# Kernel tuning notes

Measured on AMD Instinct MI355X. Metric: run time of the kernel, lower is better.

## Reference

```python
import jax, jax.numpy as jnp
import numpy as np

B, S, D = 64, 512, 512  # bias broadcast and final bmm force S == input_dim == dim_v
DK, DV = 512, 512


def setup_inputs() -> dict:
    key = jax.random.key(0)
    ks = jax.random.split(key, 16)
    sc = 0.02
    inp = {
        "sent_emb": jax.random.normal(ks[0], (B, S, D), jnp.float32),
        "pos_emb": jax.random.normal(ks[1], (B, S, D), jnp.float32),
        "branch_emb": jax.random.normal(ks[2], (B, S, D), jnp.float32),
        # Linear weights stored torch-style: [out, in]
        "Wq": jax.random.normal(ks[3], (DK, D), jnp.float32) * sc,
        "bq": jnp.zeros((DK,), jnp.float32),
        "Wk": jax.random.normal(ks[4], (DK, D), jnp.float32) * sc,
        "bk": jnp.zeros((DK,), jnp.float32),
        "Wv": jax.random.normal(ks[5], (DV, D), jnp.float32) * sc,
        "bv": jnp.zeros((DV,), jnp.float32),
        "Wpq": jax.random.normal(ks[6], (D, D), jnp.float32) * sc,
        "bpq": jnp.zeros((D,), jnp.float32),
        "Wpk": jax.random.normal(ks[7], (D, D), jnp.float32) * sc,
        "bpk": jnp.zeros((D,), jnp.float32),
        "bias": jax.random.normal(ks[8], (D,), jnp.float32) * sc,
    }
    return inp


def reference(sent_emb, pos_emb, branch_emb, Wq, bq, Wk, bk, Wv, bv, Wpq, bpq, Wpk, bpk, bias):
    d = sent_emb.shape[-1]
    norm = 1.0 / jnp.sqrt(jnp.asarray(2.0 * d, sent_emb.dtype))
    # projections (torch Linear: x @ W.T + b)
    Q = sent_emb @ Wq.T + bq          # [B,S,DK]
    K = sent_emb @ Wk.T + bk          # [B,S,DK]
    V = sent_emb @ Wv.T + bv          # [B,S,DV]
    Uq = pos_emb @ Wpq.T + bpq        # [B,S,D]
    Uk = pos_emb @ Wpk.T + bpk        # [B,S,D]
    text_score = jnp.einsum('bsd,btd->bst', Q, K) * norm   # [B,S,S]
    pos_score = jnp.einsum('bsd,btd->bst', Uq, Uk) * norm  # [B,S,S]
    att = text_score + pos_score + bias                    # bias [D] broadcasts over last axis (S==D)
    att_softmax = jax.nn.softmax(att, axis=2)
    # torch.bmm(att, V.permute(0,2,1)): out[b,i,j] = sum_t att[b,i,t] * V[b,j,t]
    output = jnp.einsum('bit,bjt->bij', att_softmax, V)    # [B,S,S] (DV==S)
    return (att_softmax, output)
```

## Files before the change

### kernel.cpp

```cpp
#include <hip/hip_runtime.h>

typedef unsigned short u16;
typedef unsigned int   u32;
typedef __bf16 bf16x8 __attribute__((ext_vector_type(8)));
typedef float  f32x4  __attribute__((ext_vector_type(4)));

#define BATCH 64
#define SEQ   512
#define BSS   (64 * 512 * 512)
#define MTOT  (64 * 512)

__device__ __forceinline__ u16 f2bf(float f) {
  u32 u = __builtin_bit_cast(u32, f);
  u += 0x7FFFu + ((u >> 16) & 1u);
  return (u16)(u >> 16);
}

__device__ __forceinline__ void gl16(const void* g, void* l) {
  __builtin_amdgcn_global_load_lds(
      (__attribute__((address_space(1))) void*)g,
      (__attribute__((address_space(3))) void*)l,
      16, 0, 0);
}

__global__ __launch_bounds__(256) void cvt2_bf16_kernel(
    const float* __restrict__ in0, u16* __restrict__ out0,
    const float* __restrict__ in1, u16* __restrict__ out1, int n8) {
  int i = blockIdx.x * 256 + threadIdx.x;
  const float* in = in0;
  u16* out = out0;
  if (i >= n8) { i -= n8; in = in1; out = out1; }
  const float4* p = reinterpret_cast<const float4*>(in) + (size_t)i * 2;
  float4 x = p[0], y = p[1];
  uint4 r;
  r.x = (u32)f2bf(x.x) | ((u32)f2bf(x.y) << 16);
  r.y = (u32)f2bf(x.z) | ((u32)f2bf(x.w) << 16);
  r.z = (u32)f2bf(y.x) | ((u32)f2bf(y.y) << 16);
  r.w = (u32)f2bf(y.z) | ((u32)f2bf(y.w) << 16);
  reinterpret_cast<uint4*>(out)[i] = r;
}

__global__ __launch_bounds__(256) void pack_w_kernel(
    const float* __restrict__ wq, const float* __restrict__ wk,
    const float* __restrict__ wv, const float* __restrict__ wpq,
    const float* __restrict__ wpk, u16* __restrict__ wc1, u16* __restrict__ wc2) {
  int i = blockIdx.x * 256 + threadIdx.x;
  int which = i >> 18;
  int off = i & 262143;
  const float* src = which == 0 ? wq : which == 1 ? wk : which == 2 ? wv
                   : which == 3 ? wpq : wpk;
  u16 h = f2bf(src[off]);
  if (which < 3) wc1[(size_t)which * 262144 + off] = h;
  else           wc2[(size_t)(which - 3) * 262144 + off] = h;
}

__global__ __launch_bounds__(256) void pack_bias_kernel(
    const float* __restrict__ bq, const float* __restrict__ bk,
    const float* __restrict__ bv, const float* __restrict__ bpq,
    const float* __restrict__ bpk, float* __restrict__ b1, float* __restrict__ b2) {
  int i = blockIdx.x * 256 + threadIdx.x;
  if (i < 1536) {
    b1[i] = i < 512 ? bq[i] : i < 1024 ? bk[i - 512] : bv[i - 1024];
  } else {
    int j = i - 1536;
    b2[j] = j < 512 ? bpq[j] : bpk[j - 512];
  }
}

template <int MODE>
__global__ __launch_bounds__(512, 2) void gemm256(
    const u16* __restrict__ A, const u16* __restrict__ Bm,
    u16* __restrict__ U0, u16* __restrict__ U1, u16* __restrict__ U2,
    const float* __restrict__ bias, float* __restrict__ F) {
  __shared__ u16 lsA[256 * 32];
  __shared__ u16 lsB[128 * 32];

  const int t = threadIdx.x;
  const int z = blockIdx.z;
  const int m0 = blockIdx.y * 256;
  const int n0 = blockIdx.x * 128;
  const int K = 512;

  const u16* Ab = A + (MODE == 2 ? (size_t)z * 262144 : 0);
  const u16* Bb = Bm + (MODE == 2 ? (size_t)z * 262144 : 0);
  float* Fb = (MODE == 2) ? (F + (size_t)z * 262144) : F;

  const int srow = t >> 2;
  const int scol = (t & 3) * 8;
  const u16* gA = Ab + (size_t)(m0 + srow) * K + scol;
  const u16* gB = Bb + (size_t)(n0 + srow) * K + scol;
  const size_t rskip = (size_t)128 * K;
  u16* lA0 = lsA + t * 8;
  u16* lA1 = lsA + 4096 + t * 8;
  u16* lB0 = lsB + t * 8;

  const int l = t & 63;
  const int w = t >> 6;
  const int wm = (w & 3) * 64;
  const int wn = (w >> 2) * 64;
  const int fr = l & 15;
  const int fk = (l >> 4) * 8;

  f32x4 acc[4][4];
#pragma unroll
  for (int i = 0; i < 4; ++i)
#pragma unroll
    for (int j = 0; j < 4; ++j) acc[i][j] = (f32x4){0.f, 0.f, 0.f, 0.f};

  for (int k0 = 0; k0 < K; k0 += 32) {
    gl16(gA + k0, lA0);
    gl16(gA + rskip + k0, lA1);
    gl16(gB + k0, lB0);
    __syncthreads();
    bf16x8 af[4], bfg[4];
#pragma unroll
    for (int mt = 0; mt < 4; ++mt)
      af[mt] = *reinterpret_cast<const bf16x8*>(&lsA[(wm + mt * 16 + fr) * 32 + fk]);
#pragma unroll
    for (int nt = 0; nt < 4; ++nt)
      bfg[nt] = *reinterpret_cast<const bf16x8*>(&lsB[(wn + nt * 16 + fr) * 32 + fk]);
#pragma unroll
    for (int mt = 0; mt < 4; ++mt)
#pragma unroll
      for (int nt = 0; nt < 4; ++nt)
        acc[mt][nt] = __builtin_amdgcn_mfma_f32_16x16x32_bf16(
            af[mt], bfg[nt], acc[mt][nt], 0, 0, 0);
    __syncthreads();
  }

  const int cr = (l >> 4) * 4;
  const int cc = l & 15;
#pragma unroll
  for (int mt = 0; mt < 4; ++mt) {
#pragma unroll
    for (int nt = 0; nt < 4; ++nt) {
      const int col = n0 + wn + nt * 16 + cc;
#pragma unroll
      for (int r = 0; r < 4; ++r) {
        const int row = m0 + wm + mt * 16 + cr + r;
        float v = acc[mt][nt][r];
        if (MODE == 2) {
          Fb[(size_t)row * 512 + col] = v;
        } else {
          v += bias[col];
          u16 h = f2bf(v);
          const int which = col >> 9, c = col & 511;
          if (MODE == 0) {
            if (which == 0)      U0[(size_t)row * 1024 + c] = h;
            else if (which == 1) U1[(size_t)row * 1024 + c] = h;
            else                 U2[(size_t)row * 512 + c] = h;
          } else {
            if (which == 0) U0[(size_t)row * 1024 + 512 + c] = h;
            else            U1[(size_t)row * 1024 + 512 + c] = h;
          }
        }
      }
    }
  }
}

__global__ __launch_bounds__(512, 4) void score_softmax(
    const u16* __restrict__ QU, const u16* __restrict__ KU,
    const float* __restrict__ bias, float* __restrict__ attF,
    u16* __restrict__ attB) {
  __shared__ u16 lsA[64 * 256];
  __shared__ float sred[64 * 8];

  const int t = threadIdx.x;
  const int b = blockIdx.x;
  const int rg = blockIdx.y;
  const int l = t & 63;
  const int w = t >> 6;
  const int wn = w * 64;
  const int fr = l & 15;
  const int fkb = (l >> 4) * 16;
  const int cc = l & 15;
  const int cr = (l >> 4) * 4;
  const int sw = (l & 7) << 4;

  const int browA = b * 512 + rg * 64;

  const int stg_colb = ((t & 31) << 4) ^ (((t >> 5) & 7) << 4);
  const char* gAc = (const char*)QU + (size_t)(browA + (t >> 5)) * 2048 + stg_colb;

  const u16* gK = KU + (size_t)(b * 512 + wn + fr) * 1024 + (l >> 4) * 8;

  float bc[4];
#pragma unroll
  for (int nt = 0; nt < 4; ++nt) bc[nt] = bias[wn + nt * 16 + cc];

  f32x4 acc[4][4];
#pragma unroll
  for (int i = 0; i < 4; ++i)
#pragma unroll
    for (int j = 0; j < 4; ++j) acc[i][j] = (f32x4){0.f, 0.f, 0.f, 0.f};

#pragma unroll
  for (int c = 0; c < 4; ++c) {
    __syncthreads();
#pragma unroll
    for (int i = 0; i < 4; ++i)
      gl16(gAc + c * 512 + (size_t)i * 16 * 2048,
           (char*)lsA + t * 16 + (size_t)i * 8192);
    __syncthreads();

#pragma unroll 2
    for (int kk = 0; kk < 8; ++kk) {
      bf16x8 af[4], bfg[4];
#pragma unroll
      for (int nt = 0; nt < 4; ++nt)
        bfg[nt] = *reinterpret_cast<const bf16x8*>(
            gK + (size_t)nt * 16 * 1024 + c * 256 + kk * 32);
#pragma unroll
      for (int mt = 0; mt < 4; ++mt)
        af[mt] = *reinterpret_cast<const bf16x8*>(
            (const char*)lsA + (mt * 16 + fr) * 512 + ((kk * 64 + fkb) ^ sw));
#pragma unroll
      for (int mt = 0; mt < 4; ++mt)
#pragma unroll
        for (int nt = 0; nt < 4; ++nt)
          acc[mt][nt] = __builtin_amdgcn_mfma_f32_16x16x32_bf16(
              af[mt], bfg[nt], acc[mt][nt], 0, 0, 0);
    }
  }

#pragma unroll
  for (int mt = 0; mt < 4; ++mt)
#pragma unroll
    for (int nt = 0; nt < 4; ++nt)
#pragma unroll
      for (int r = 0; r < 4; ++r)
        acc[mt][nt][r] = acc[mt][nt][r] * 0.03125f + bc[nt];

  float rm[4][4];
#pragma unroll
  for (int mt = 0; mt < 4; ++mt)
#pragma unroll
    for (int r = 0; r < 4; ++r) {
      float m = fmaxf(fmaxf(acc[mt][0][r], acc[mt][1][r]),
                      fmaxf(acc[mt][2][r], acc[mt][3][r]));
#pragma unroll
      for (int s = 1; s < 16; s <<= 1) m = fmaxf(m, __shfl_xor(m, s, 64));
      rm[mt][r] = m;
    }
  if (cc == 0) {
#pragma unroll
    for (int mt = 0; mt < 4; ++mt)
#pragma unroll
      for (int r = 0; r < 4; ++r)
        sred[(mt * 16 + cr + r) * 8 + w] = rm[mt][r];
  }
  __syncthreads();
#pragma unroll
  for (int mt = 0; mt < 4; ++mt)
#pragma unroll
    for (int r = 0; r < 4; ++r) {
      const float* p = &sred[(mt * 16 + cr + r) * 8];
      f32x4 a = *reinterpret_cast<const f32x4*>(p);
      f32x4 c = *reinterpret_cast<const f32x4*>(p + 4);
      rm[mt][r] = fmaxf(fmaxf(fmaxf(a[0], a[1]), fmaxf(a[2], a[3])),
                        fmaxf(fmaxf(c[0], c[1]), fmaxf(c[2], c[3])));
    }
  __syncthreads();

  float rs[4][4];
#pragma unroll
  for (int mt = 0; mt < 4; ++mt)
#pragma unroll
    for (int r = 0; r < 4; ++r) {
      float s = 0.f;
#pragma unroll
      for (int nt = 0; nt < 4; ++nt) {
        float e = __expf(acc[mt][nt][r] - rm[mt][r]);
        acc[mt][nt][r] = e;
        s += e;
      }
#pragma unroll
      for (int sh = 1; sh < 16; sh <<= 1) s += __shfl_xor(s, sh, 64);
      rs[mt][r] = s;
    }
  if (cc == 0) {
#pragma unroll
    for (int mt = 0; mt < 4; ++mt)
#pragma unroll
      for (int r = 0; r < 4; ++r)
        sred[(mt * 16 + cr + r) * 8 + w] = rs[mt][r];
  }
  __syncthreads();
#pragma unroll
  for (int mt = 0; mt < 4; ++mt)
#pragma unroll
    for (int r = 0; r < 4; ++r) {
      const float* p = &sred[(mt * 16 + cr + r) * 8];
      f32x4 a = *reinterpret_cast<const f32x4*>(p);
      f32x4 c = *reinterpret_cast<const f32x4*>(p + 4);
      rs[mt][r] = 1.0f / ((a[0] + a[1]) + (a[2] + a[3]) +
                          (c[0] + c[1]) + (c[2] + c[3]));
    }

  float* aF = attF + (size_t)b * 262144 + (size_t)rg * 64 * 512;
  u16* aB = attB + (size_t)b * 262144 + (size_t)rg * 64 * 512;
#pragma unroll
  for (int mt = 0; mt < 4; ++mt)
#pragma unroll
    for (int nt = 0; nt < 4; ++nt)
#pragma unroll
      for (int r = 0; r < 4; ++r) {
        const size_t idx = (size_t)(mt * 16 + cr + r) * 512 + wn + nt * 16 + cc;
        float a = acc[mt][nt][r] * rs[mt][r];
        aF[idx] = a;
        aB[idx] = f2bf(a);
      }
}

extern "C" void kernel_launch(void* const* d_in, const int* in_sizes, int n_in,
                              void* d_out, int out_size, void* d_ws,
                              size_t ws_size, hipStream_t stream) {
  const float* sent = (const float*)d_in[0];
  const float* pos  = (const float*)d_in[1];
  const float* Wq  = (const float*)d_in[3];
  const float* bq  = (const float*)d_in[4];
  const float* Wk  = (const float*)d_in[5];
  const float* bk  = (const float*)d_in[6];
  const float* Wv  = (const float*)d_in[7];
  const float* bv  = (const float*)d_in[8];
  const float* Wpq = (const float*)d_in[9];
  const float* bpq = (const float*)d_in[10];
  const float* Wpk = (const float*)d_in[11];
  const float* bpk = (const float*)d_in[12];
  const float* abias = (const float*)d_in[13];
  float* out = (float*)d_out;

  char* ws = (char*)d_ws;
  u16* Xs   = (u16*)(ws);
  u16* Xp   = (u16*)(ws + 33554432ul);
  u16* QU   = (u16*)(ws + 67108864ul);
  u16* KU   = (u16*)(ws + 134217728ul);
  u16* Vb   = (u16*)(ws + 201326592ul);
  u16* attB = (u16*)(ws + 234881024ul);
  u16* Wc1  = (u16*)(ws + 268435456ul);
  u16* Wc2  = (u16*)(ws + 270008320ul);
  float* b1 = (float*)(ws + 271056896ul);
  float* b2 = (float*)(ws + 271063040ul);

  float* attF = out;
  float* out2 = out + BSS;

  cvt2_bf16_kernel<<<16384, 256, 0, stream>>>(sent, Xs, pos, Xp, MTOT * 512 / 8);
  pack_w_kernel<<<5120, 256, 0, stream>>>(Wq, Wk, Wv, Wpq, Wpk, Wc1, Wc2);
  pack_bias_kernel<<<10, 256, 0, stream>>>(bq, bk, bv, bpq, bpk, b1, b2);

  gemm256<0><<<dim3(12, 128, 1), 512, 0, stream>>>(Xs, Wc1, QU, KU, Vb, b1, nullptr);
  gemm256<1><<<dim3(8, 128, 1), 512, 0, stream>>>(Xp, Wc2, QU, KU, nullptr, b2, nullptr);

  score_softmax<<<dim3(BATCH, 8, 1), 512, 0, stream>>>(QU, KU, abias, attF, attB);

  gemm256<2><<<dim3(4, 2, BATCH), 512, 0, stream>>>(attB, Vb, nullptr, nullptr,
                                                    nullptr, nullptr, out2);

  (void)in_sizes; (void)n_in; (void)out_size; (void)ws_size;
}
```

Measured before the change: 542.9 us.

## Replace LDS-staged GEMM with barrier-free direct global-to-register MFMA loads

Result: slower. 766.3 us (+41.1%).

```diff
diff --git a/kernel.cpp b/kernel.cpp
--- a/kernel.cpp
+++ b/kernel.cpp
@@ -68,38 +68,28 @@
 }
 
 template <int MODE>
-__global__ __launch_bounds__(512, 2) void gemm256(
+__global__ __launch_bounds__(256, 2) void gemm_bfree(
     const u16* __restrict__ A, const u16* __restrict__ Bm,
     u16* __restrict__ U0, u16* __restrict__ U1, u16* __restrict__ U2,
     const float* __restrict__ bias, float* __restrict__ F) {
-  __shared__ u16 lsA[256 * 32];
-  __shared__ u16 lsB[128 * 32];
-
   const int t = threadIdx.x;
   const int z = blockIdx.z;
-  const int m0 = blockIdx.y * 256;
+  const int m0 = blockIdx.y * 128;
   const int n0 = blockIdx.x * 128;
-  const int K = 512;
 
   const u16* Ab = A + (MODE == 2 ? (size_t)z * 262144 : 0);
   const u16* Bb = Bm + (MODE == 2 ? (size_t)z * 262144 : 0);
   float* Fb = (MODE == 2) ? (F + (size_t)z * 262144) : F;
 
-  const int srow = t >> 2;
-  const int scol = (t & 3) * 8;
-  const u16* gA = Ab + (size_t)(m0 + srow) * K + scol;
-  const u16* gB = Bb + (size_t)(n0 + srow) * K + scol;
-  const size_t rskip = (size_t)128 * K;
-  u16* lA0 = lsA + t * 8;
-  u16* lA1 = lsA + 4096 + t * 8;
-  u16* lB0 = lsB + t * 8;
-
   const int l = t & 63;
   const int w = t >> 6;
-  const int wm = (w & 3) * 64;
-  const int wn = (w >> 2) * 64;
+  const int wm = (w & 1) * 64;
+  const int wn = (w >> 1) * 64;
   const int fr = l & 15;
-  const int fk = (l >> 4) * 8;
+  const int fo = (l >> 4) * 8;
+
+  const u16* gA = Ab + (size_t)(m0 + wm + fr) * 512 + fo;
+  const u16* gB = Bb + (size_t)(n0 + wn + fr) * 512 + fo;
 
   f32x4 acc[4][4];
 #pragma unroll
@@ -107,25 +97,38 @@
 #pragma unroll
     for (int j = 0; j < 4; ++j) acc[i][j] = (f32x4){0.f, 0.f, 0.f, 0.f};
 
-  for (int k0 = 0; k0 < K; k0 += 32) {
-    gl16(gA + k0, lA0);
-    gl16(gA + rskip + k0, lA1);
-    gl16(gB + k0, lB0);
-    __syncthreads();
-    bf16x8 af[4], bfg[4];
-#pragma unroll
-    for (int mt = 0; mt < 4; ++mt)
-      af[mt] = *reinterpret_cast<const bf16x8*>(&lsA[(wm + mt * 16 + fr) * 32 + fk]);
-#pragma unroll
-    for (int nt = 0; nt < 4; ++nt)
-      bfg[nt] = *reinterpret_cast<const bf16x8*>(&lsB[(wn + nt * 16 + fr) * 32 + fk]);
+  bf16x8 a0[4], b0[4], a1[4], b1[4];
+#pragma unroll
+  for (int i = 0; i < 4; ++i) {
+    a0[i] = *reinterpret_cast<const bf16x8*>(gA + (size_t)i * 16 * 512);
+    b0[i] = *reinterpret_cast<const bf16x8*>(gB + (size_t)i * 16 * 512);
+  }
+
+  for (int k0 = 0; k0 < 512; k0 += 64) {
+    const int k1 = k0 + 32;
+    const int k2 = (k0 + 64) & 511;
+#pragma unroll
+    for (int i = 0; i < 4; ++i) {
+      a1[i] = *reinterpret_cast<const bf16x8*>(gA + (size_t)i * 16 * 512 + k1);
+      b1[i] = *reinterpret_cast<const bf16x8*>(gB + (size_t)i * 16 * 512 + k1);
+    }
 #pragma unroll
     for (int mt = 0; mt < 4; ++mt)
 #pragma unroll
       for (int nt = 0; nt < 4; ++nt)
         acc[mt][nt] = __builtin_amdgcn_mfma_f32_16x16x32_bf16(
-            af[mt], bfg[nt], acc[mt][nt], 0, 0, 0);
-    __syncthreads();
+            a0[mt], b0[nt], acc[mt][nt], 0, 0, 0);
+#pragma unroll
+    for (int i = 0; i < 4; ++i) {
+      a0[i] = *reinterpret_cast<const bf16x8*>(gA + (size_t)i * 16 * 512 + k2);
+      b0[i] = *reinterpret_cast<const bf16x8*>(gB + (size_t)i * 16 * 512 + k2);
+    }
+#pragma unroll
+    for (int mt = 0; mt < 4; ++mt)
+#pragma unroll
+      for (int nt = 0; nt < 4; ++nt)
+        acc[mt][nt] = __builtin_amdgcn_mfma_f32_16x16x32_bf16(
+            a1[mt], b1[nt], acc[mt][nt], 0, 0, 0);
   }
 
   const int cr = (l >> 4) * 4;
@@ -350,13 +353,13 @@
   pack_w_kernel<<<5120, 256, 0, stream>>>(Wq, Wk, Wv, Wpq, Wpk, Wc1, Wc2);
   pack_bias_kernel<<<10, 256, 0, stream>>>(bq, bk, bv, bpq, bpk, b1, b2);
 
-  gemm256<0><<<dim3(12, 128, 1), 512, 0, stream>>>(Xs, Wc1, QU, KU, Vb, b1, nullptr);
-  gemm256<1><<<dim3(8, 128, 1), 512, 0, stream>>>(Xp, Wc2, QU, KU, nullptr, b2, nullptr);
+  gemm_bfree<0><<<dim3(12, 256, 1), 256, 0, stream>>>(Xs, Wc1, QU, KU, Vb, b1, nullptr);
+  gemm_bfree<1><<<dim3(8, 256, 1), 256, 0, stream>>>(Xp, Wc2, QU, KU, nullptr, b2, nullptr);
 
   score_softmax<<<dim3(BATCH, 8, 1), 512, 0, stream>>>(QU, KU, abias, attF, attB);
 
-  gemm256<2><<<dim3(4, 2, BATCH), 512, 0, stream>>>(attB, Vb, nullptr, nullptr,
-                                                    nullptr, nullptr, out2);
+  gemm_bfree<2><<<dim3(4, 4, BATCH), 256, 0, stream>>>(attB, Vb, nullptr, nullptr,
+                                                       nullptr, nullptr, out2);
 
   (void)in_sizes; (void)n_in; (void)out_size; (void)ws_size;
 }
```

## Double-buffer GEMM LDS tiles with XOR swizzle and XCD-aware block remap

Applied to the files above, without the earlier changes.

Result: faster. 504.0 us (-7.2%).

```diff
diff --git a/kernel.cpp b/kernel.cpp
--- a/kernel.cpp
+++ b/kernel.cpp
@@ -68,38 +68,46 @@
 }
 
 template <int MODE>
-__global__ __launch_bounds__(512, 2) void gemm256(
+__global__ __launch_bounds__(512, 4) void gemm_db(
     const u16* __restrict__ A, const u16* __restrict__ Bm,
     u16* __restrict__ U0, u16* __restrict__ U1, u16* __restrict__ U2,
     const float* __restrict__ bias, float* __restrict__ F) {
-  __shared__ u16 lsA[256 * 32];
-  __shared__ u16 lsB[128 * 32];
+  __shared__ u16 ls[2 * 12288];
 
   const int t = threadIdx.x;
-  const int z = blockIdx.z;
-  const int m0 = blockIdx.y * 256;
-  const int n0 = blockIdx.x * 128;
+
+  const int gx = gridDim.x, gy = gridDim.y;
+  int id = (blockIdx.z * gy + blockIdx.y) * gx + blockIdx.x;
+  const int q = (gx * gy * gridDim.z) >> 3;
+  id = (id & 7) * q + (id >> 3);
+  const int bx = id % gx;
+  const int rem = id / gx;
+  const int by = rem % gy;
+  const int z = rem / gy;
+
+  const int m0 = by * 256;
+  const int n0 = bx * 128;
   const int K = 512;
 
   const u16* Ab = A + (MODE == 2 ? (size_t)z * 262144 : 0);
   const u16* Bb = Bm + (MODE == 2 ? (size_t)z * 262144 : 0);
   float* Fb = (MODE == 2) ? (F + (size_t)z * 262144) : F;
 
-  const int srow = t >> 2;
-  const int scol = (t & 3) * 8;
+  const int u = (t & 7) ^ ((t >> 3) & 7);
+  const int srow = 2 * (t >> 3) + (u & 1);
+  const int scol = (u >> 1) * 8;
   const u16* gA = Ab + (size_t)(m0 + srow) * K + scol;
   const u16* gB = Bb + (size_t)(n0 + srow) * K + scol;
-  const size_t rskip = (size_t)128 * K;
-  u16* lA0 = lsA + t * 8;
-  u16* lA1 = lsA + 4096 + t * 8;
-  u16* lB0 = lsB + t * 8;
 
   const int l = t & 63;
   const int w = t >> 6;
   const int wm = (w & 3) * 64;
   const int wn = (w >> 2) * 64;
   const int fr = l & 15;
-  const int fk = (l >> 4) * 8;
+
+  const int sOff = ((2 * (l >> 4) + (fr & 1)) ^ (fr >> 1)) << 4;
+  const int aoffB = (((wm + fr) & ~1) << 6) + sOff;
+  const int boffB = 16384 + (((wn + fr) & ~1) << 6) + sOff;
 
   f32x4 acc[4][4];
 #pragma unroll
@@ -107,25 +115,39 @@
 #pragma unroll
     for (int j = 0; j < 4; ++j) acc[i][j] = (f32x4){0.f, 0.f, 0.f, 0.f};
 
-  for (int k0 = 0; k0 < K; k0 += 32) {
-    gl16(gA + k0, lA0);
-    gl16(gA + rskip + k0, lA1);
-    gl16(gB + k0, lB0);
-    __syncthreads();
-    bf16x8 af[4], bfg[4];
+  {
+    char* Ld = (char*)ls + t * 16;
+    gl16(gA, Ld);
+    gl16(gA + (size_t)128 * K, Ld + 8192);
+    gl16(gB, Ld + 16384);
+  }
+  __syncthreads();
+
+  int cur = 0;
+  for (int it = 0; it < 16; ++it) {
+    if (it < 15) {
+      const int k0 = (it + 1) * 32;
+      char* Ld = (char*)ls + (cur ^ 1) * 24576 + t * 16;
+      gl16(gA + k0, Ld);
+      gl16(gA + (size_t)128 * K + k0, Ld + 8192);
+      gl16(gB + k0, Ld + 16384);
+    }
+    const char* Lc = (const char*)ls + cur * 24576;
+    bf16x8 af[4], bfv[4];
 #pragma unroll
     for (int mt = 0; mt < 4; ++mt)
-      af[mt] = *reinterpret_cast<const bf16x8*>(&lsA[(wm + mt * 16 + fr) * 32 + fk]);
+      af[mt] = *reinterpret_cast<const bf16x8*>(Lc + aoffB + mt * 1024);
 #pragma unroll
     for (int nt = 0; nt < 4; ++nt)
-      bfg[nt] = *reinterpret_cast<const bf16x8*>(&lsB[(wn + nt * 16 + fr) * 32 + fk]);
+      bfv[nt] = *reinterpret_cast<const bf16x8*>(Lc + boffB + nt * 1024);
 #pragma unroll
     for (int mt = 0; mt < 4; ++mt)
 #pragma unroll
       for (int nt = 0; nt < 4; ++nt)
         acc[mt][nt] = __builtin_amdgcn_mfma_f32_16x16x32_bf16(
-            af[mt], bfg[nt], acc[mt][nt], 0, 0, 0);
+            af[mt], bfv[nt], acc[mt][nt], 0, 0, 0);
     __syncthreads();
+    cur ^= 1;
   }
 
   const int cr = (l >> 4) * 4;
@@ -350,12 +372,12 @@
   pack_w_kernel<<<5120, 256, 0, stream>>>(Wq, Wk, Wv, Wpq, Wpk, Wc1, Wc2);
   pack_bias_kernel<<<10, 256, 0, stream>>>(bq, bk, bv, bpq, bpk, b1, b2);
 
-  gemm256<0><<<dim3(12, 128, 1), 512, 0, stream>>>(Xs, Wc1, QU, KU, Vb, b1, nullptr);
-  gemm256<1><<<dim3(8, 128, 1), 512, 0, stream>>>(Xp, Wc2, QU, KU, nullptr, b2, nullptr);
+  gemm_db<0><<<dim3(12, 128, 1), 512, 0, stream>>>(Xs, Wc1, QU, KU, Vb, b1, nullptr);
+  gemm_db<1><<<dim3(8, 128, 1), 512, 0, stream>>>(Xp, Wc2, QU, KU, nullptr, b2, nullptr);
 
   score_softmax<<<dim3(BATCH, 8, 1), 512, 0, stream>>>(QU, KU, abias, attF, attB);
 
-  gemm256<2><<<dim3(4, 2, BATCH), 512, 0, stream>>>(attB, Vb, nullptr, nullptr,
+  gemm_db<2><<<dim3(4, 2, BATCH), 512, 0, stream>>>(attB, Vb, nullptr, nullptr,
                                                     nullptr, nullptr, out2);
 
   (void)in_sizes; (void)n_in; (void)out_size; (void)ws_size;
```
